# Kernel tuning notes

Hardware: AMD Instinct MI355X
Metric: run time of the kernel (lower is better)

Reference implementation:

```python
import jax, jax.numpy as jnp
import numpy as np

B, G, NPA, NT, L = 8192, 689, 16, 131, 6
S = G + NPA * NT  # 2785 = 689 genes + 16 nodes per each of 131 assemblies


def setup_inputs() -> dict:
    key = jax.random.key(0)
    ks = jax.random.split(key, 8)
    x = jax.random.normal(ks[0], (B, G), dtype=jnp.float32)
    # depth-0 mask: place the 689 gene inputs into the first 689 slots of the layer
    lm0 = jnp.zeros((G, S), jnp.float32).at[jnp.arange(G), jnp.arange(G)].set(1.0)
    # per-depth sparse binary connectivity masks (ontology DAG edges at each depth)
    lm = (jax.random.uniform(ks[1], (L, S, S)) < 0.02).astype(jnp.float32)
    # diagonal pass-through masks for edges skipping this depth (stored as diagonals)
    flm_diag = (jax.random.uniform(ks[2], (L, S)) < 0.3).astype(jnp.float32)
    # final assembly selector: the nodes_per_assembly slots of the root assembly
    fasm = jnp.zeros((S,), jnp.float32).at[G:G + NPA].set(1.0)
    W0 = jax.random.normal(ks[3], (G, S), dtype=jnp.float32) * 0.05
    b0 = jnp.zeros((S,), jnp.float32)
    W = jax.random.normal(ks[4], (L, S, S), dtype=jnp.float32) * 0.05
    b = jnp.zeros((L, S), jnp.float32)
    gamma = jnp.ones((L + 1, S), jnp.float32)
    beta = jnp.zeros((L + 1, S), jnp.float32)
    w_out = jax.random.normal(ks[5], (S,), dtype=jnp.float32) * 0.05
    b_out = jnp.zeros((), jnp.float32)
    return {"x": x, "lm0": lm0, "lm": lm, "flm_diag": flm_diag, "fasm": fasm,
            "W0": W0, "b0": b0, "W": W, "b": b, "gamma": gamma, "beta": beta,
            "w_out": w_out, "b_out": b_out}


def _bn(h, g, bt, eps=1e-5):
    # training-mode BatchNorm1d over the batch axis
    m = h.mean(axis=0)
    v = h.var(axis=0)
    return (h - m) * jax.lax.rsqrt(v + eps) * g + bt


def reference(x, lm0, lm, flm_diag, fasm, W0, b0, W, b, gamma, beta, w_out, b_out):
    # depth 0: masked linear placing genes into layer slots, BN before activation
    h = jnp.tanh(_bn(x @ (W0 * lm0) + b0, gamma[0], beta[0]))  # [B, S]
    def step(h, layer):
        Wl, bl, lml, dl, gl, btl = layer
        # masked linear + BN + activation, plus diagonal pass-through skip
        hn = jnp.tanh(_bn(h @ (Wl * lml) + bl, gl, btl)) + h * dl
        return hn, None
    h, _ = jax.lax.scan(step, h, (W, b, lm, flm_diag, gamma[1:], beta[1:]))
    # output_method='final': linear head on final-assembly nodes only
    return (h * fasm) @ w_out + b_out  # [B]
```

## Files before the change

### kernel.cpp

```cpp
#include <hip/hip_runtime.h>
#include <hip/hip_fp16.h>
#include <stdint.h>

typedef uint32_t u32;
typedef uint64_t u64;
typedef unsigned int v4u __attribute__((ext_vector_type(4)));
typedef float v4f __attribute__((ext_vector_type(4)));
typedef _Float16 v2h __attribute__((ext_vector_type(2)));

constexpr int CB   = 8192;
constexpr int CG   = 689;
constexpr int CL   = 6;
constexpr int CS   = 2785;
constexpr int CSP  = 2816;
constexpr int CRS  = 8256;
constexpr int KCAP = 112;
constexpr int TILE = 32;
constexpr int NTIL = 88;

union V16 { v4u u; v2h h2[4]; };
union F4  { v4f v; float f[4]; u32 u[4]; };
union HW  { u32 u; v2h h; };

__global__ __launch_bounds__(256) void build_tables(const float* __restrict__ lm0,
                                                    const float* __restrict__ W0,
                                                    const float* __restrict__ lm,
                                                    const float* __restrict__ W,
                                                    u64* __restrict__ ent,
                                                    int* __restrict__ cnt)
{
    __shared__ u64 eL[TILE * KCAP];
    __shared__ int cL[TILE];

    int tbl  = blockIdx.y;
    int x    = blockIdx.x;
    int tile = (x & 7) * (NTIL / 8) + (x >> 3);
    int s0   = tile * TILE;

    const float* mbase; const float* wbase; int nrows;
    if (tbl == 0) { mbase = lm0; wbase = W0; nrows = CG; }
    else {
        size_t off = (size_t)(tbl - 1) * CS * CS;
        mbase = lm + off; wbase = W + off; nrows = CS;
    }

    int t = threadIdx.x;
    for (int i = t; i < TILE * KCAP; i += 256) eL[i] = 0;
    if (t < TILE) cL[t] = 0;
    __syncthreads();

    int rl = t >> 3;
    int cq = (t & 7) * 4;
    int c  = s0 + cq;
    int np = (nrows + 31) >> 5;

    for (int p = 0; p < np; p++) {
        int r = p * 32 + rl;
        if (r >= nrows) continue;
        const float* mr = mbase + (size_t)r * CS;
        if (c + 3 < CS) {
            F4 m4; m4.v = *reinterpret_cast<const v4f*>(mr + c);
            if ((m4.u[0] | m4.u[1] | m4.u[2] | m4.u[3]) == 0u) continue;
            F4 w4; w4.v = *reinterpret_cast<const v4f*>(wbase + (size_t)r * CS + c);
            u64 hi = ((u64)((u32)r * (u32)(CRS * 2))) << 32;
#pragma unroll
            for (int q = 0; q < 4; q++) {
                if (m4.f[q] != 0.0f) {
                    int pos = atomicAdd(&cL[cq + q], 1);
                    if (pos < KCAP) {
                        u32 hw = (u32)__half_as_ushort(__float2half(w4.f[q]));
                        eL[(cq + q) * KCAP + pos] = hi | (u64)(hw | (hw << 16));
                    }
                }
            }
        } else {
            u64 hi = ((u64)((u32)r * (u32)(CRS * 2))) << 32;
            for (int q = 0; q < 4; q++) {
                int cc = c + q;
                if (cc >= CS) break;
                float m = mr[cc];
                if (m != 0.0f) {
                    int pos = atomicAdd(&cL[cq + q], 1);
                    if (pos < KCAP) {
                        u32 hw = (u32)__half_as_ushort(__float2half(wbase[(size_t)r * CS + cc]));
                        eL[(cq + q) * KCAP + pos] = hi | (u64)(hw | (hw << 16));
                    }
                }
            }
        }
    }
    __syncthreads();

    size_t gbase = (size_t)(tbl * CSP + s0) * KCAP;
    for (int i = t; i < TILE * KCAP; i += 256)
        ent[gbase + i] = eL[i];
    if (t < TILE) {
        int n = cL[t]; if (n > KCAP) n = KCAP;
        cnt[tbl * CSP + s0 + t] = n;
    }
}

__global__ __launch_bounds__(256) void transpose_x(const float* __restrict__ x,
                                                   __half* __restrict__ xT)
{
    __shared__ float tile[32][33];
    int gx = blockIdx.x * 32;
    int gy = blockIdx.y * 32;
    int tx = threadIdx.x, ty = threadIdx.y;
#pragma unroll
    for (int i = 0; i < 32; i += 8) {
        int g = gx + tx;
        int b = gy + ty + i;
        tile[ty + i][tx] = (g < CG) ? x[(size_t)b * CG + g] : 0.f;
    }
    __syncthreads();
#pragma unroll
    for (int i = 0; i < 32; i += 8) {
        int g = gx + ty + i;
        int b = gy + tx;
        if (g < CG) xT[(size_t)g * CRS + b] = __float2half(tile[tx][ty + i]);
    }
}

__global__ __launch_bounds__(64) void gather_k(const __half* __restrict__ src,
                                               __half* __restrict__ dst,
                                               const u64* __restrict__ ent,
                                               const int* __restrict__ cnt,
                                               const float* __restrict__ bias,
                                               float* __restrict__ sumv,
                                               float* __restrict__ sumq,
                                               const int* __restrict__ sel,
                                               const int* __restrict__ selcnt)
{
    int s;
    if (sel) {
        if ((int)blockIdx.y >= *selcnt) return;
        s = sel[blockIdx.y];
    } else {
        s = blockIdx.y;
    }
    int lane = threadIdx.x;
    int boff = blockIdx.z * 4096 + blockIdx.x * 512 + lane * 8;

    int n = cnt[s]; if (n > KCAP) n = KCAP;
    int ng = (n + 7) >> 3;
    const u64* e = ent + (size_t)s * KCAP;
    const char* sb = (const char*)src + (size_t)boff * 2;

    float bv = bias[s];
    float acc[8];
#pragma unroll
    for (int j = 0; j < 8; j++) acc[j] = bv;

    for (int g = 0; g < ng; g++) {
        u64 ev[8];
#pragma unroll
        for (int q = 0; q < 8; q++) ev[q] = e[g * 8 + q];
        V16 rv[8];
#pragma unroll
        for (int q = 0; q < 8; q++)
            rv[q].u = *reinterpret_cast<const v4u*>(sb + (u32)(ev[q] >> 32));
#pragma unroll
        for (int q = 0; q < 8; q++) {
            HW w2; w2.u = (u32)ev[q];
#pragma unroll
            for (int j = 0; j < 4; j++) {
                float2 f = __half22float2(*(const __half2*)&rv[q].h2[j]);
                float w = __half2float(*(const __half*)&w2.h);
                acc[2*j]   = fmaf(w, f.x, acc[2*j]);
                acc[2*j+1] = fmaf(w, f.y, acc[2*j+1]);
            }
        }
    }

    V16 o;
#pragma unroll
    for (int j = 0; j < 4; j++) {
        v2h p; p.x = (_Float16)acc[2*j]; p.y = (_Float16)acc[2*j+1];
        o.h2[j] = p;
    }
    __builtin_nontemporal_store(o.u, reinterpret_cast<v4u*>(dst + (size_t)s * CRS + boff));

    float ls = 0.f, lq = 0.f;
#pragma unroll
    for (int j = 0; j < 8; j++) { ls += acc[j]; lq += acc[j] * acc[j]; }
#pragma unroll
    for (int off = 32; off > 0; off >>= 1) {
        ls += __shfl_xor(ls, off);
        lq += __shfl_xor(lq, off);
    }
    if (lane == 0) { atomicAdd(&sumv[s], ls); atomicAdd(&sumq[s], lq); }
}

__global__ __launch_bounds__(64) void bn_act(__half* __restrict__ h,
                                             const __half* __restrict__ prev,
                                             const float* __restrict__ sumv,
                                             const float* __restrict__ sumq,
                                             const float* __restrict__ gamma,
                                             const float* __restrict__ beta,
                                             const float* __restrict__ dlv)
{
    int s = blockIdx.y;
    int boff = blockIdx.x * 512 + threadIdx.x * 8;
    float mean = sumv[s] * (1.0f / CB);
    float var  = sumq[s] * (1.0f / CB) - mean * mean;
    float rstd = rsqrtf(var + 1e-5f);
    float scale = gamma[s] * rstd;
    float shift = beta[s] - mean * scale;
    size_t base = (size_t)s * CRS + boff;
    V16 v; v.u = *reinterpret_cast<const v4u*>(h + base);
    V16 pv;
    float d = 0.f;
    if (prev) { d = dlv[s]; pv.u = *reinterpret_cast<const v4u*>(prev + base); }
    V16 o;
#pragma unroll
    for (int j = 0; j < 4; j++) {
        float2 f = __half22float2(*(const __half2*)&v.h2[j]);
        float t0 = tanhf(fmaf(f.x, scale, shift));
        float t1 = tanhf(fmaf(f.y, scale, shift));
        if (prev) {
            float2 p = __half22float2(*(const __half2*)&pv.h2[j]);
            t0 = fmaf(d, p.x, t0);
            t1 = fmaf(d, p.y, t1);
        }
        v2h pk; pk.x = (_Float16)t0; pk.y = (_Float16)t1;
        o.h2[j] = pk;
    }
    *reinterpret_cast<v4u*>(h + base) = o.u;
}

__global__ __launch_bounds__(256) void head_prep(const float* __restrict__ fasm,
                                                 const float* __restrict__ wout,
                                                 int* __restrict__ hcnt,
                                                 int* __restrict__ hs,
                                                 float* __restrict__ hc)
{
    int s = blockIdx.x * 256 + threadIdx.x;
    if (s >= CS) return;
    float c = fasm[s] * wout[s];
    if (c != 0.f) {
        int p = atomicAdd(hcnt, 1);
        if (p < 64) { hs[p] = s; hc[p] = c; }
    }
}

__global__ __launch_bounds__(256) void head_k(const __half* __restrict__ h6pre,
                                              const __half* __restrict__ h5,
                                              const int* __restrict__ hcnt,
                                              const int* __restrict__ hs,
                                              const float* __restrict__ hc,
                                              const float* __restrict__ sumv,
                                              const float* __restrict__ sumq,
                                              const float* __restrict__ gamma,
                                              const float* __restrict__ beta,
                                              const float* __restrict__ dlv,
                                              const float* __restrict__ bout,
                                              float* __restrict__ out)
{
    int b = blockIdx.x * 256 + threadIdx.x;
    int n = *hcnt; if (n > 64) n = 64;
    float acc = bout[0];
    for (int k = 0; k < n; k++) {
        int s = hs[k];
        float mean = sumv[s] * (1.0f / CB);
        float var  = sumq[s] * (1.0f / CB) - mean * mean;
        float rstd = rsqrtf(var + 1e-5f);
        float scale = gamma[s] * rstd;
        float shift = beta[s] - mean * scale;
        float pre  = __half2float(h6pre[(size_t)s * CRS + b]);
        float prev = __half2float(h5[(size_t)s * CRS + b]);
        float hn = tanhf(fmaf(pre, scale, shift)) + dlv[s] * prev;
        acc = fmaf(hc[k], hn, acc);
    }
    out[b] = acc;
}

extern "C" void kernel_launch(void* const* d_in, const int* in_sizes, int n_in,
                              void* d_out, int out_size, void* d_ws, size_t ws_size,
                              hipStream_t stream)
{
    const float* x    = (const float*)d_in[0];
    const float* lm0  = (const float*)d_in[1];
    const float* lm   = (const float*)d_in[2];
    const float* flm  = (const float*)d_in[3];
    const float* fasm = (const float*)d_in[4];
    const float* W0   = (const float*)d_in[5];
    const float* b0   = (const float*)d_in[6];
    const float* W    = (const float*)d_in[7];
    const float* bb   = (const float*)d_in[8];
    const float* gam  = (const float*)d_in[9];
    const float* bet  = (const float*)d_in[10];
    const float* wout = (const float*)d_in[11];
    const float* bout = (const float*)d_in[12];
    float* out = (float*)d_out;

    char* ws = (char*)d_ws;
    int*    cnt  = (int*)ws;
    float*  sumv = (float*)(ws + 78848);
    float*  sumq = (float*)(ws + 157696);
    int*    hcnt = (int*)(ws + 236544);
    int*    hs   = (int*)(ws + 236560);
    float*  hc   = (float*)(ws + 236816);
    u64*    ent  = (u64*)(ws + 237184);
    __half* hA   = (__half*)(ws + 17899136);
    __half* hB   = (__half*)(ws + 63885056);
    __half* xT   = hB;

    (void)hipMemsetAsync(ws + 78848, 0, 158224, stream);

    build_tables<<<dim3(NTIL, 7), 256, 0, stream>>>(lm0, W0, lm, W, ent, cnt);
    transpose_x<<<dim3(22, 256), dim3(32, 8), 0, stream>>>(x, xT);
    head_prep<<<dim3(11), 256, 0, stream>>>(fasm, wout, hcnt, hs, hc);

    const __half* cur = xT;
    __half* bufs[2] = {hA, hB};
    int which = 0;
    for (int t = 0; t < 6; t++) {
        __half* dst = bufs[which];
        const float* bias = (t == 0) ? b0 : bb + (size_t)(t - 1) * CS;
        gather_k<<<dim3(8, CS, 2), 64, 0, stream>>>(cur, dst,
            ent + (size_t)t * CSP * KCAP, cnt + t * CSP, bias,
            sumv + t * CSP, sumq + t * CSP, nullptr, nullptr);
        bn_act<<<dim3(16, CS), 64, 0, stream>>>(dst, (t == 0) ? nullptr : cur,
            sumv + t * CSP, sumq + t * CSP, gam + (size_t)t * CS, bet + (size_t)t * CS,
            (t == 0) ? nullptr : flm + (size_t)(t - 1) * CS);
        cur = dst;
        which ^= 1;
    }
    __half* h6 = bufs[which];
    gather_k<<<dim3(8, 16, 2), 64, 0, stream>>>(cur, h6,
        ent + (size_t)6 * CSP * KCAP, cnt + 6 * CSP, bb + (size_t)5 * CS,
        sumv + 6 * CSP, sumq + 6 * CSP, hs, hcnt);
    head_k<<<dim3(32), 256, 0, stream>>>(h6, cur, hcnt, hs, hc,
        sumv + 6 * CSP, sumq + 6 * CSP, gam + (size_t)6 * CS, bet + (size_t)6 * CS,
        flm + (size_t)5 * CS, bout, out);
}
```

Measured before the change: 1.193 ms.

## Split sparse table build across row slices with atomic global append

The mask-scanning table builder now splits the row range of each column tile into 8 slices launched as separate blocks, so 8x more workgroups stream the large dense mask and weight matrices in parallel. Each slice collects entries in a smaller shared buffer and appends them into the global per-column list through an atomic counter. The whole workspace (counts and entry table) is now zeroed by a larger memset instead of by the kernel. Entry order within a column becomes nondeterministic, and a per-slice cap of 40 could in principle drop entries.

Result: no change. 1.170 ms (-1.9%).

```diff
diff --git a/kernel.cpp b/kernel.cpp
--- a/kernel.cpp
+++ b/kernel.cpp
@@ -17,6 +17,8 @@
 constexpr int KCAP = 112;
 constexpr int TILE = 32;
 constexpr int NTIL = 88;
+constexpr int RSPL = 8;
+constexpr int LCAP = 40;
 
 union V16 { v4u u; v2h h2[4]; };
 union F4  { v4f v; float f[4]; u32 u[4]; };
@@ -29,13 +31,15 @@
                                                     u64* __restrict__ ent,
                                                     int* __restrict__ cnt)
 {
-    __shared__ u64 eL[TILE * KCAP];
+    __shared__ u64 eL[TILE * LCAP];
     __shared__ int cL[TILE];
-
-    int tbl  = blockIdx.y;
-    int x    = blockIdx.x;
-    int tile = (x & 7) * (NTIL / 8) + (x >> 3);
-    int s0   = tile * TILE;
+    __shared__ int bL[TILE];
+
+    int tbl   = blockIdx.z;
+    int slice = blockIdx.y;
+    int x     = blockIdx.x;
+    int tile  = (x & 7) * (NTIL / 8) + (x >> 3);
+    int s0    = tile * TILE;
 
     const float* mbase; const float* wbase; int nrows;
     if (tbl == 0) { mbase = lm0; wbase = W0; nrows = CG; }
@@ -43,20 +47,20 @@
         size_t off = (size_t)(tbl - 1) * CS * CS;
         mbase = lm + off; wbase = W + off; nrows = CS;
     }
+    int r0 = slice * nrows / RSPL;
+    int r1 = (slice + 1) * nrows / RSPL;
 
     int t = threadIdx.x;
-    for (int i = t; i < TILE * KCAP; i += 256) eL[i] = 0;
     if (t < TILE) cL[t] = 0;
     __syncthreads();
 
     int rl = t >> 3;
     int cq = (t & 7) * 4;
     int c  = s0 + cq;
-    int np = (nrows + 31) >> 5;
-
-    for (int p = 0; p < np; p++) {
-        int r = p * 32 + rl;
-        if (r >= nrows) continue;
+
+    for (int p = r0; p < r1; p += 32) {
+        int r = p + rl;
+        if (r >= r1) continue;
         const float* mr = mbase + (size_t)r * CS;
         if (c + 3 < CS) {
             F4 m4; m4.v = *reinterpret_cast<const v4f*>(mr + c);
@@ -67,9 +71,9 @@
             for (int q = 0; q < 4; q++) {
                 if (m4.f[q] != 0.0f) {
                     int pos = atomicAdd(&cL[cq + q], 1);
-                    if (pos < KCAP) {
+                    if (pos < LCAP) {
                         u32 hw = (u32)__half_as_ushort(__float2half(w4.f[q]));
-                        eL[(cq + q) * KCAP + pos] = hi | (u64)(hw | (hw << 16));
+                        eL[(cq + q) * LCAP + pos] = hi | (u64)(hw | (hw << 16));
                     }
                 }
             }
@@ -81,9 +85,9 @@
                 float m = mr[cc];
                 if (m != 0.0f) {
                     int pos = atomicAdd(&cL[cq + q], 1);
-                    if (pos < KCAP) {
+                    if (pos < LCAP) {
                         u32 hw = (u32)__half_as_ushort(__float2half(wbase[(size_t)r * CS + cc]));
-                        eL[(cq + q) * KCAP + pos] = hi | (u64)(hw | (hw << 16));
+                        eL[(cq + q) * LCAP + pos] = hi | (u64)(hw | (hw << 16));
                     }
                 }
             }
@@ -91,12 +95,16 @@
     }
     __syncthreads();
 
-    size_t gbase = (size_t)(tbl * CSP + s0) * KCAP;
-    for (int i = t; i < TILE * KCAP; i += 256)
-        ent[gbase + i] = eL[i];
-    if (t < TILE) {
-        int n = cL[t]; if (n > KCAP) n = KCAP;
-        cnt[tbl * CSP + s0 + t] = n;
+    int col = t >> 3, sub = t & 7;
+    int gc  = tbl * CSP + s0 + col;
+    int n = cL[col]; if (n > LCAP) n = LCAP;
+    if (sub == 0) bL[col] = atomicAdd(&cnt[gc], n);
+    __syncthreads();
+    int base = bL[col];
+    u64* eg = ent + (size_t)gc * KCAP;
+    for (int i = sub; i < n; i += 8) {
+        int pos = base + i;
+        if (pos < KCAP) eg[pos] = eL[col * LCAP + i];
     }
 }
 
@@ -306,9 +314,9 @@
     __half* hB   = (__half*)(ws + 63885056);
     __half* xT   = hB;
 
-    (void)hipMemsetAsync(ws + 78848, 0, 158224, stream);
-
-    build_tables<<<dim3(NTIL, 7), 256, 0, stream>>>(lm0, W0, lm, W, ent, cnt);
+    (void)hipMemsetAsync(ws, 0, 17899136, stream);
+
+    build_tables<<<dim3(NTIL, RSPL, 7), 256, 0, stream>>>(lm0, W0, lm, W, ent, cnt);
     transpose_x<<<dim3(22, 256), dim3(32, 8), 0, stream>>>(x, xT);
     head_prep<<<dim3(11), 256, 0, stream>>>(fasm, wout, hcnt, hs, hc);
 
```
